# Kernel optimization log

Hardware: AMD Instinct MI355X
Metric: run time of the kernel (lower is better)

## Reference

```python
import jax, jax.numpy as jnp
import numpy as np
from jax import lax

T = 1.0      # terminal time
SIGMA = 1.0  # diffusion coefficient
N, D, P, M, H = 16384, 16, 8, 50, 128


def setup_inputs() -> dict:
    key = jax.random.key(0)
    ks = jax.random.split(key, 8)
    scale1 = 1.0 / np.sqrt(1 + D + P)
    scale2 = 1.0 / np.sqrt(H)
    return {
        "initial_states": jax.random.normal(ks[0], (N, D), jnp.float32),
        "initial_values": jax.random.normal(ks[1], (N,), jnp.float32),
        "observations": jax.random.normal(ks[2], (N, P), jnp.float32),
        "noise": jax.random.normal(ks[3], (M, N, D), jnp.float32),
        "W1": jax.random.normal(ks[4], (1 + D + P, H), jnp.float32) * scale1,
        "b1": jnp.zeros((H,), jnp.float32),
        "W2": jax.random.normal(ks[5], (H, H), jnp.float32) * scale2,
        "b2": jnp.zeros((H,), jnp.float32),
        "W3": jax.random.normal(ks[6], (H, D), jnp.float32) * scale2,
        "b3": jnp.zeros((D,), jnp.float32),
    }


def reference(initial_states, initial_values, observations, noise,
              W1, b1, W2, b2, W3, b3):
    """Euler-Maruyama rollout of simulate_SDEs: joint (X, V) SDE with
    per-step Z-network drift. drift b(X) = -X (OU process)."""
    m_steps = noise.shape[0]
    dt = jnp.asarray(T / m_steps, initial_states.dtype)
    sqrt_dt = jnp.sqrt(dt)
    times = jnp.arange(m_steps, dtype=initial_states.dtype) * dt  # time[m]

    def z_net(t, X, Y):
        tcol = jnp.full((X.shape[0], 1), t, X.dtype)
        h = jnp.concatenate([tcol, X, Y], axis=1)      # (N, 1+d+p)
        h = jax.nn.relu(h @ W1 + b1)
        h = jax.nn.relu(h @ W2 + b2)
        return h @ W3 + b3                             # (N, d)

    def step(carry, inp):
        X, V = carry
        eps, t = inp
        Wn = sqrt_dt * eps                             # Brownian increment
        Z = z_net(t, X, observations)
        drift_V = 0.5 * jnp.sum(Z * Z, axis=1)
        V = V + dt * drift_V + jnp.sum(Z * Wn, axis=1)
        X = X + dt * (-X) + SIGMA * Wn                 # b(X) = -X
        return (X, V), None

    (X, V), _ = lax.scan(step, (initial_states, initial_values), (noise, times))
    return X, V
```

## Files before the change

### kernel.cpp

```cpp
#include <hip/hip_runtime.h>

typedef __bf16   bf16x8 __attribute__((ext_vector_type(8)));
typedef float    f32x4  __attribute__((ext_vector_type(4)));
typedef float    f32x2  __attribute__((ext_vector_type(2)));
typedef uint32_t u32x4  __attribute__((ext_vector_type(4)));

constexpr int N_ = 16384;
constexpr int D_ = 16;
constexpr int P_ = 8;
constexpr int H_ = 128;
constexpr int M_ = 50;

__device__ __forceinline__ uint32_t pk_bf16(float a, float b) {
    uint32_t ua = __builtin_bit_cast(uint32_t, a) + 0x8000u;
    uint32_t ub = __builtin_bit_cast(uint32_t, b) + 0x8000u;
    return __builtin_amdgcn_perm(ub, ua, 0x07060302u);
}
__device__ __forceinline__ uint32_t pk_relu_bf16(float a, float b) {
    return pk_bf16(fmaxf(a, 0.0f), fmaxf(b, 0.0f));
}

__global__ __launch_bounds__(64, 1)
void sde_fused(const float* __restrict__ X0,
               const float* __restrict__ V0,
               const float* __restrict__ Yobs,
               const float* __restrict__ noise,
               const float* __restrict__ W1, const float* __restrict__ b1,
               const float* __restrict__ W2, const float* __restrict__ b2,
               const float* __restrict__ W3, const float* __restrict__ b3,
               float* __restrict__ out)
{
    const int lane = threadIdx.x;
    const int n    = lane & 15;
    const int q    = lane >> 4;
    const int gr   = blockIdx.x * 16 + n;

    const float dt   = 0.02f;
    const float sqdt = 0.1414213562373095f;

    bf16x8 w1f[8];
#pragma unroll
    for (int ct = 0; ct < 8; ++ct) {
        u32x4 u;
        u[0] = pk_bf16(W1[(1 + q * 4 + 0) * H_ + ct * 16 + n],
                       W1[(1 + q * 4 + 1) * H_ + ct * 16 + n]);
        u[1] = pk_bf16(W1[(1 + q * 4 + 2) * H_ + ct * 16 + n],
                       W1[(1 + q * 4 + 3) * H_ + ct * 16 + n]);
        u[2] = pk_bf16(W1[(17 + q * 2 + 0) * H_ + ct * 16 + n],
                       W1[(17 + q * 2 + 1) * H_ + ct * 16 + n]);
        u[3] = (q == 0) ? pk_bf16(b1[ct * 16 + n], W1[ct * 16 + n]) : 0u;
        w1f[ct] = __builtin_bit_cast(bf16x8, u);
    }
    bf16x8 w2f[8][4];
#pragma unroll
    for (int ct = 0; ct < 8; ++ct)
#pragma unroll
        for (int kt = 0; kt < 4; ++kt) {
            u32x4 u;
#pragma unroll
            for (int w = 0; w < 4; ++w) {
                int h0 = (kt * 2 + (w >> 1)) * 16 + q * 4 + (w & 1) * 2;
                u[w] = pk_bf16(W2[h0 * H_ + ct * 16 + n],
                               W2[(h0 + 1) * H_ + ct * 16 + n]);
            }
            w2f[ct][kt] = __builtin_bit_cast(bf16x8, u);
        }
    bf16x8 w3f[4];
#pragma unroll
    for (int kt = 0; kt < 4; ++kt) {
        u32x4 u;
#pragma unroll
        for (int w = 0; w < 4; ++w) {
            int h0 = (kt * 2 + (w >> 1)) * 16 + q * 4 + (w & 1) * 2;
            u[w] = pk_bf16(W3[h0 * D_ + n], W3[(h0 + 1) * D_ + n]);
        }
        w3f[kt] = __builtin_bit_cast(bf16x8, u);
    }
    f32x4 b2r[8];
#pragma unroll
    for (int ct = 0; ct < 8; ++ct)
#pragma unroll
        for (int r = 0; r < 4; ++r) b2r[ct][r] = b2[ct * 16 + q * 4 + r];
    f32x4 b3r;
#pragma unroll
    for (int r = 0; r < 4; ++r) b3r[r] = b3[q * 4 + r];

    f32x4 x = *(const f32x4*)&X0[gr * D_ + q * 4];
    f32x2 y2 = *(const f32x2*)&Yobs[gr * P_ + q * 2];
    const uint32_t yw = pk_bf16(y2[0], y2[1]);

    const float* npb = noise + (size_t)gr * D_ + q * 4;
    f32x4 e0 = *(const f32x4*)npb;
    f32x4 e1 = *(const f32x4*)(npb + (size_t)N_ * D_);
    float t = 0.0f;
    float vacc = 0.0f;

    for (int m = 0; m < M_; ++m) {
        int mp = (m + 2 < M_) ? (m + 2) : (M_ - 1);
        f32x4 e2 = *(const f32x4*)(npb + (size_t)mp * N_ * D_);

        u32x4 au;
        au[0] = pk_bf16(x[0], x[1]);
        au[1] = pk_bf16(x[2], x[3]);
        au[2] = yw;
        au[3] = (q == 0) ? pk_bf16(1.0f, t) : 0u;
        bf16x8 a0 = __builtin_bit_cast(bf16x8, au);

        f32x4 h1c[8];
#pragma unroll
        for (int ct = 0; ct < 8; ++ct)
            h1c[ct] = __builtin_amdgcn_mfma_f32_16x16x32_bf16(
                w1f[ct], a0, (f32x4){0.f, 0.f, 0.f, 0.f}, 0, 0, 0);

        bf16x8 h1b[4];
#pragma unroll
        for (int kt = 0; kt < 4; ++kt) {
            u32x4 u;
            u[0] = pk_relu_bf16(h1c[2 * kt][0], h1c[2 * kt][1]);
            u[1] = pk_relu_bf16(h1c[2 * kt][2], h1c[2 * kt][3]);
            u[2] = pk_relu_bf16(h1c[2 * kt + 1][0], h1c[2 * kt + 1][1]);
            u[3] = pk_relu_bf16(h1c[2 * kt + 1][2], h1c[2 * kt + 1][3]);
            h1b[kt] = __builtin_bit_cast(bf16x8, u);
        }

        f32x4 h2c[8];
#pragma unroll
        for (int ct = 0; ct < 8; ++ct) {
            f32x4 c = b2r[ct];
#pragma unroll
            for (int kt = 0; kt < 4; ++kt)
                c = __builtin_amdgcn_mfma_f32_16x16x32_bf16(w2f[ct][kt], h1b[kt], c, 0, 0, 0);
            h2c[ct] = c;
        }
        bf16x8 h2b[4];
#pragma unroll
        for (int kt = 0; kt < 4; ++kt) {
            u32x4 u;
            u[0] = pk_relu_bf16(h2c[2 * kt][0], h2c[2 * kt][1]);
            u[1] = pk_relu_bf16(h2c[2 * kt][2], h2c[2 * kt][3]);
            u[2] = pk_relu_bf16(h2c[2 * kt + 1][0], h2c[2 * kt + 1][1]);
            u[3] = pk_relu_bf16(h2c[2 * kt + 1][2], h2c[2 * kt + 1][3]);
            h2b[kt] = __builtin_bit_cast(bf16x8, u);
        }

        f32x4 za = __builtin_amdgcn_mfma_f32_16x16x32_bf16(w3f[0], h2b[0], b3r, 0, 0, 0);
        za = __builtin_amdgcn_mfma_f32_16x16x32_bf16(w3f[1], h2b[1], za, 0, 0, 0);
        f32x4 zb = __builtin_amdgcn_mfma_f32_16x16x32_bf16(
            w3f[2], h2b[2], (f32x4){0.f, 0.f, 0.f, 0.f}, 0, 0, 0);
        zb = __builtin_amdgcn_mfma_f32_16x16x32_bf16(w3f[3], h2b[3], zb, 0, 0, 0);

#pragma unroll
        for (int r = 0; r < 4; ++r) {
            float z  = za[r] + zb[r];
            float wn = sqdt * e0[r];
            vacc = fmaf(z, wn, fmaf(0.01f * z, z, vacc));
            x[r] = fmaf(x[r], 0.98f, wn);
        }

        e0 = e1; e1 = e2;
        t += dt;
    }

    float part = vacc;
    part += __shfl_xor(part, 16);
    part += __shfl_xor(part, 32);
    float v = V0[gr] + part;

    *(f32x4*)&out[gr * D_ + q * 4] = x;
    if (q == 0) out[N_ * D_ + gr] = v;
}

extern "C" void kernel_launch(void* const* d_in, const int* in_sizes, int n_in,
                              void* d_out, int out_size, void* d_ws, size_t ws_size,
                              hipStream_t stream)
{
    const float* X0 = (const float*)d_in[0];
    const float* V0 = (const float*)d_in[1];
    const float* Y  = (const float*)d_in[2];
    const float* nz = (const float*)d_in[3];
    const float* W1 = (const float*)d_in[4];
    const float* b1 = (const float*)d_in[5];
    const float* W2 = (const float*)d_in[6];
    const float* b2 = (const float*)d_in[7];
    const float* W3 = (const float*)d_in[8];
    const float* b3 = (const float*)d_in[9];
    float* out = (float*)d_out;

    sde_fused<<<N_ / 16, 64, 0, stream>>>(X0, V0, Y, nz, W1, b1, W2, b2, W3, b3, out);
}
```

Before: 139.6 us.

## Split hidden dimension across two waves with LDS exchange between MLP layers

Each 16-row block now uses two waves instead of one. Each wave computes half of the hidden columns for layers 1 and 2, then the halves are swapped through shared memory with a barrier so both waves hold full activations. This halves the per-wave MFMA chain and weight-register footprint, which is meant to cut per-step latency and raise occupancy. In exchange it adds two barriers and LDS round trips per time step, and both waves redundantly run layer 3 and the state update.

Measured after the change: 147.3 us. 1.06x slower.

```diff
diff --git a/kernel.cpp b/kernel.cpp
--- a/kernel.cpp
+++ b/kernel.cpp
@@ -20,7 +20,7 @@
     return pk_bf16(fmaxf(a, 0.0f), fmaxf(b, 0.0f));
 }
 
-__global__ __launch_bounds__(64, 1)
+__global__ __launch_bounds__(128, 2)
 void sde_fused(const float* __restrict__ X0,
                const float* __restrict__ V0,
                const float* __restrict__ Yobs,
@@ -30,17 +30,22 @@
                const float* __restrict__ W3, const float* __restrict__ b3,
                float* __restrict__ out)
 {
-    const int lane = threadIdx.x;
+    const int tid  = threadIdx.x;
+    const int lane = tid & 63;
+    const int wv   = tid >> 6;
     const int n    = lane & 15;
     const int q    = lane >> 4;
     const int gr   = blockIdx.x * 16 + n;
 
+    const int ct0 = wv * 4;
+
     const float dt   = 0.02f;
     const float sqdt = 0.1414213562373095f;
 
-    bf16x8 w1f[8];
-#pragma unroll
-    for (int ct = 0; ct < 8; ++ct) {
+    bf16x8 w1f[4];
+#pragma unroll
+    for (int c = 0; c < 4; ++c) {
+        const int ct = ct0 + c;
         u32x4 u;
         u[0] = pk_bf16(W1[(1 + q * 4 + 0) * H_ + ct * 16 + n],
                        W1[(1 + q * 4 + 1) * H_ + ct * 16 + n]);
@@ -49,41 +54,47 @@
         u[2] = pk_bf16(W1[(17 + q * 2 + 0) * H_ + ct * 16 + n],
                        W1[(17 + q * 2 + 1) * H_ + ct * 16 + n]);
         u[3] = (q == 0) ? pk_bf16(b1[ct * 16 + n], W1[ct * 16 + n]) : 0u;
-        w1f[ct] = __builtin_bit_cast(bf16x8, u);
-    }
-    bf16x8 w2f[8][4];
-#pragma unroll
-    for (int ct = 0; ct < 8; ++ct)
-#pragma unroll
-        for (int kt = 0; kt < 4; ++kt) {
+        w1f[c] = __builtin_bit_cast(bf16x8, u);
+    }
+    bf16x8 w2f[4][4];
+#pragma unroll
+    for (int cc = 0; cc < 4; ++cc) {
+        const int ct = ct0 + cc;
+#pragma unroll
+        for (int s = 0; s < 4; ++s) {
+            const int g = (s < 2) ? (2 * wv + s) : (2 * (wv ^ 1) + (s - 2));
             u32x4 u;
 #pragma unroll
             for (int w = 0; w < 4; ++w) {
-                int h0 = (kt * 2 + (w >> 1)) * 16 + q * 4 + (w & 1) * 2;
+                int h0 = (g * 2 + (w >> 1)) * 16 + q * 4 + (w & 1) * 2;
                 u[w] = pk_bf16(W2[h0 * H_ + ct * 16 + n],
                                W2[(h0 + 1) * H_ + ct * 16 + n]);
             }
-            w2f[ct][kt] = __builtin_bit_cast(bf16x8, u);
-        }
+            w2f[cc][s] = __builtin_bit_cast(bf16x8, u);
+        }
+    }
     bf16x8 w3f[4];
 #pragma unroll
-    for (int kt = 0; kt < 4; ++kt) {
+    for (int s = 0; s < 4; ++s) {
+        const int g = (s < 2) ? (2 * wv + s) : (2 * (wv ^ 1) + (s - 2));
         u32x4 u;
 #pragma unroll
         for (int w = 0; w < 4; ++w) {
-            int h0 = (kt * 2 + (w >> 1)) * 16 + q * 4 + (w & 1) * 2;
+            int h0 = (g * 2 + (w >> 1)) * 16 + q * 4 + (w & 1) * 2;
             u[w] = pk_bf16(W3[h0 * D_ + n], W3[(h0 + 1) * D_ + n]);
         }
-        w3f[kt] = __builtin_bit_cast(bf16x8, u);
-    }
-    f32x4 b2r[8];
-#pragma unroll
-    for (int ct = 0; ct < 8; ++ct)
-#pragma unroll
-        for (int r = 0; r < 4; ++r) b2r[ct][r] = b2[ct * 16 + q * 4 + r];
+        w3f[s] = __builtin_bit_cast(bf16x8, u);
+    }
+    f32x4 b2r[4];
+#pragma unroll
+    for (int cc = 0; cc < 4; ++cc)
+#pragma unroll
+        for (int r = 0; r < 4; ++r) b2r[cc][r] = b2[(ct0 + cc) * 16 + q * 4 + r];
     f32x4 b3r;
 #pragma unroll
     for (int r = 0; r < 4; ++r) b3r[r] = b3[q * 4 + r];
+
+    __shared__ bf16x8 xch[2][2][2][64];
 
     f32x4 x = *(const f32x4*)&X0[gr * D_ + q * 4];
     f32x2 y2 = *(const f32x2*)&Yobs[gr * P_ + q * 2];
@@ -106,48 +117,80 @@
         au[3] = (q == 0) ? pk_bf16(1.0f, t) : 0u;
         bf16x8 a0 = __builtin_bit_cast(bf16x8, au);
 
-        f32x4 h1c[8];
-#pragma unroll
-        for (int ct = 0; ct < 8; ++ct)
-            h1c[ct] = __builtin_amdgcn_mfma_f32_16x16x32_bf16(
-                w1f[ct], a0, (f32x4){0.f, 0.f, 0.f, 0.f}, 0, 0, 0);
-
-        bf16x8 h1b[4];
-#pragma unroll
-        for (int kt = 0; kt < 4; ++kt) {
-            u32x4 u;
-            u[0] = pk_relu_bf16(h1c[2 * kt][0], h1c[2 * kt][1]);
-            u[1] = pk_relu_bf16(h1c[2 * kt][2], h1c[2 * kt][3]);
-            u[2] = pk_relu_bf16(h1c[2 * kt + 1][0], h1c[2 * kt + 1][1]);
-            u[3] = pk_relu_bf16(h1c[2 * kt + 1][2], h1c[2 * kt + 1][3]);
-            h1b[kt] = __builtin_bit_cast(bf16x8, u);
-        }
-
-        f32x4 h2c[8];
-#pragma unroll
-        for (int ct = 0; ct < 8; ++ct) {
-            f32x4 c = b2r[ct];
-#pragma unroll
-            for (int kt = 0; kt < 4; ++kt)
-                c = __builtin_amdgcn_mfma_f32_16x16x32_bf16(w2f[ct][kt], h1b[kt], c, 0, 0, 0);
-            h2c[ct] = c;
-        }
-        bf16x8 h2b[4];
-#pragma unroll
-        for (int kt = 0; kt < 4; ++kt) {
-            u32x4 u;
-            u[0] = pk_relu_bf16(h2c[2 * kt][0], h2c[2 * kt][1]);
-            u[1] = pk_relu_bf16(h2c[2 * kt][2], h2c[2 * kt][3]);
-            u[2] = pk_relu_bf16(h2c[2 * kt + 1][0], h2c[2 * kt + 1][1]);
-            u[3] = pk_relu_bf16(h2c[2 * kt + 1][2], h2c[2 * kt + 1][3]);
-            h2b[kt] = __builtin_bit_cast(bf16x8, u);
-        }
-
-        f32x4 za = __builtin_amdgcn_mfma_f32_16x16x32_bf16(w3f[0], h2b[0], b3r, 0, 0, 0);
-        za = __builtin_amdgcn_mfma_f32_16x16x32_bf16(w3f[1], h2b[1], za, 0, 0, 0);
+        f32x4 h1c[4];
+#pragma unroll
+        for (int c = 0; c < 4; ++c)
+            h1c[c] = __builtin_amdgcn_mfma_f32_16x16x32_bf16(
+                w1f[c], a0, (f32x4){0.f, 0.f, 0.f, 0.f}, 0, 0, 0);
+
+        bf16x8 my0, my1;
+        {
+            u32x4 u;
+            u[0] = pk_relu_bf16(h1c[0][0], h1c[0][1]);
+            u[1] = pk_relu_bf16(h1c[0][2], h1c[0][3]);
+            u[2] = pk_relu_bf16(h1c[1][0], h1c[1][1]);
+            u[3] = pk_relu_bf16(h1c[1][2], h1c[1][3]);
+            my0 = __builtin_bit_cast(bf16x8, u);
+        }
+        {
+            u32x4 u;
+            u[0] = pk_relu_bf16(h1c[2][0], h1c[2][1]);
+            u[1] = pk_relu_bf16(h1c[2][2], h1c[2][3]);
+            u[2] = pk_relu_bf16(h1c[3][0], h1c[3][1]);
+            u[3] = pk_relu_bf16(h1c[3][2], h1c[3][3]);
+            my1 = __builtin_bit_cast(bf16x8, u);
+        }
+
+        xch[0][wv][0][lane] = my0;
+        xch[0][wv][1][lane] = my1;
+        asm volatile("s_waitcnt lgkmcnt(0)" ::: "memory");
+        __builtin_amdgcn_s_barrier();
+        __builtin_amdgcn_sched_barrier(0);
+        bf16x8 ot0 = xch[0][wv ^ 1][0][lane];
+        bf16x8 ot1 = xch[0][wv ^ 1][1][lane];
+
+        f32x4 h2c[4];
+#pragma unroll
+        for (int cc = 0; cc < 4; ++cc) {
+            f32x4 c = b2r[cc];
+            c = __builtin_amdgcn_mfma_f32_16x16x32_bf16(w2f[cc][0], my0, c, 0, 0, 0);
+            c = __builtin_amdgcn_mfma_f32_16x16x32_bf16(w2f[cc][1], my1, c, 0, 0, 0);
+            c = __builtin_amdgcn_mfma_f32_16x16x32_bf16(w2f[cc][2], ot0, c, 0, 0, 0);
+            c = __builtin_amdgcn_mfma_f32_16x16x32_bf16(w2f[cc][3], ot1, c, 0, 0, 0);
+            h2c[cc] = c;
+        }
+
+        bf16x8 m20, m21;
+        {
+            u32x4 u;
+            u[0] = pk_relu_bf16(h2c[0][0], h2c[0][1]);
+            u[1] = pk_relu_bf16(h2c[0][2], h2c[0][3]);
+            u[2] = pk_relu_bf16(h2c[1][0], h2c[1][1]);
+            u[3] = pk_relu_bf16(h2c[1][2], h2c[1][3]);
+            m20 = __builtin_bit_cast(bf16x8, u);
+        }
+        {
+            u32x4 u;
+            u[0] = pk_relu_bf16(h2c[2][0], h2c[2][1]);
+            u[1] = pk_relu_bf16(h2c[2][2], h2c[2][3]);
+            u[2] = pk_relu_bf16(h2c[3][0], h2c[3][1]);
+            u[3] = pk_relu_bf16(h2c[3][2], h2c[3][3]);
+            m21 = __builtin_bit_cast(bf16x8, u);
+        }
+
+        xch[1][wv][0][lane] = m20;
+        xch[1][wv][1][lane] = m21;
+        asm volatile("s_waitcnt lgkmcnt(0)" ::: "memory");
+        __builtin_amdgcn_s_barrier();
+        __builtin_amdgcn_sched_barrier(0);
+        bf16x8 o20 = xch[1][wv ^ 1][0][lane];
+        bf16x8 o21 = xch[1][wv ^ 1][1][lane];
+
+        f32x4 za = __builtin_amdgcn_mfma_f32_16x16x32_bf16(w3f[0], m20, b3r, 0, 0, 0);
+        za = __builtin_amdgcn_mfma_f32_16x16x32_bf16(w3f[1], m21, za, 0, 0, 0);
         f32x4 zb = __builtin_amdgcn_mfma_f32_16x16x32_bf16(
-            w3f[2], h2b[2], (f32x4){0.f, 0.f, 0.f, 0.f}, 0, 0, 0);
-        zb = __builtin_amdgcn_mfma_f32_16x16x32_bf16(w3f[3], h2b[3], zb, 0, 0, 0);
+            w3f[2], o20, (f32x4){0.f, 0.f, 0.f, 0.f}, 0, 0, 0);
+        zb = __builtin_amdgcn_mfma_f32_16x16x32_bf16(w3f[3], o21, zb, 0, 0, 0);
 
 #pragma unroll
         for (int r = 0; r < 4; ++r) {
@@ -164,10 +207,11 @@
     float part = vacc;
     part += __shfl_xor(part, 16);
     part += __shfl_xor(part, 32);
-    float v = V0[gr] + part;
-
-    *(f32x4*)&out[gr * D_ + q * 4] = x;
-    if (q == 0) out[N_ * D_ + gr] = v;
+
+    if (wv == 0) {
+        *(f32x4*)&out[gr * D_ + q * 4] = x;
+        if (q == 0) out[N_ * D_ + gr] = V0[gr] + part;
+    }
 }
 
 extern "C" void kernel_launch(void* const* d_in, const int* in_sizes, int n_in,
@@ -186,5 +230,5 @@
     const float* b3 = (const float*)d_in[9];
     float* out = (float*)d_out;
 
-    sde_fused<<<N_ / 16, 64, 0, stream>>>(X0, V0, Y, nz, W1, b1, W2, b2, W3, b3, out);
-}
+    sde_fused<<<N_ / 16, 128, 0, stream>>>(X0, V0, Y, nz, W1, b1, W2, b2, W3, b3, out);
+}
```

## Split time steps across two waves per sample group using closed-form X recurrence

Applied to the files above, without the earlier changes.

Each block now runs two wavefronts over the same 16 samples. The first handles steps 0-24. The second first replays the cheap X recurrence over the first 25 noise slices to get X at the midpoint, then runs the MLP for steps 25-49. The V partial sums are combined through shared memory, which halves the serial MLP chain per wave and doubles the number of waves available to hide MFMA latency. In exchange it reads the first half of the noise twice, adds a block barrier, and raises register pressure, since launch bounds allow two blocks of 128 threads.

After: 240.6 us. 72.4% more time.

```diff
diff --git a/kernel.cpp b/kernel.cpp
--- a/kernel.cpp
+++ b/kernel.cpp
@@ -20,7 +20,7 @@
     return pk_bf16(fmaxf(a, 0.0f), fmaxf(b, 0.0f));
 }
 
-__global__ __launch_bounds__(64, 1)
+__global__ __launch_bounds__(128, 2)
 void sde_fused(const float* __restrict__ X0,
                const float* __restrict__ V0,
                const float* __restrict__ Yobs,
@@ -30,7 +30,9 @@
                const float* __restrict__ W3, const float* __restrict__ b3,
                float* __restrict__ out)
 {
-    const int lane = threadIdx.x;
+    const int tid  = threadIdx.x;
+    const int lane = tid & 63;
+    const int half = tid >> 6;
     const int n    = lane & 15;
     const int q    = lane >> 4;
     const int gr   = blockIdx.x * 16 + n;
@@ -90,13 +92,27 @@
     const uint32_t yw = pk_bf16(y2[0], y2[1]);
 
     const float* npb = noise + (size_t)gr * D_ + q * 4;
-    f32x4 e0 = *(const f32x4*)npb;
-    f32x4 e1 = *(const f32x4*)(npb + (size_t)N_ * D_);
-    float t = 0.0f;
+
+    if (half == 1) {
+#pragma unroll 5
+        for (int m = 0; m < 25; ++m) {
+            f32x4 e = *(const f32x4*)(npb + (size_t)m * N_ * D_);
+#pragma unroll
+            for (int r = 0; r < 4; ++r)
+                x[r] = fmaf(x[r], 0.98f, sqdt * e[r]);
+        }
+    }
+
+    const int s0 = half * 25;
+    float t = half ? 0.5f : 0.0f;
+
+    f32x4 e0 = *(const f32x4*)(npb + (size_t)s0 * N_ * D_);
+    f32x4 e1 = *(const f32x4*)(npb + (size_t)(s0 + 1) * N_ * D_);
     float vacc = 0.0f;
 
-    for (int m = 0; m < M_; ++m) {
-        int mp = (m + 2 < M_) ? (m + 2) : (M_ - 1);
+    for (int i = 0; i < 25; ++i) {
+        const int m  = s0 + i;
+        const int mp = (m + 2 < M_) ? (m + 2) : (M_ - 1);
         f32x4 e2 = *(const f32x4*)(npb + (size_t)mp * N_ * D_);
 
         u32x4 au;
@@ -164,10 +180,14 @@
     float part = vacc;
     part += __shfl_xor(part, 16);
     part += __shfl_xor(part, 32);
-    float v = V0[gr] + part;
-
-    *(f32x4*)&out[gr * D_ + q * 4] = x;
-    if (q == 0) out[N_ * D_ + gr] = v;
+
+    __shared__ float vpart[16];
+    if (half == 0 && q == 0) vpart[n] = part;
+    __syncthreads();
+    if (half == 1) {
+        *(f32x4*)&out[gr * D_ + q * 4] = x;
+        if (q == 0) out[N_ * D_ + gr] = V0[gr] + vpart[n] + part;
+    }
 }
 
 extern "C" void kernel_launch(void* const* d_in, const int* in_sizes, int n_in,
@@ -186,5 +206,5 @@
     const float* b3 = (const float*)d_in[9];
     float* out = (float*)d_out;
 
-    sde_fused<<<N_ / 16, 64, 0, stream>>>(X0, V0, Y, nz, W1, b1, W2, b2, W3, b3, out);
-}
+    sde_fused<<<N_ / 16, 128, 0, stream>>>(X0, V0, Y, nz, W1, b1, W2, b2, W3, b3, out);
+}
```

## Software-pipeline layer-1 MFMA of next step and use hardware bf16 pack

Applied to the files above, without the earlier changes.

Restructures the time loop so the next step's X update and first-layer MFMAs are issued alongside the current step's layer-2/3 MFMAs. This breaks the serial dependency chain inside a single wave, since each block is only one wave with one block per launch-bound. It also replaces the manual add-and-permute bf16 packing with the v_cvt_pk_bf16_f32 instruction, which rounds to nearest even. The cost is higher register pressure from the extra h1cn accumulators, and the loop is now `unroll 1` with a peeled prologue and epilogue.

After: 139.3 us. About the same (-0.2%).

```diff
diff --git a/kernel.cpp b/kernel.cpp
--- a/kernel.cpp
+++ b/kernel.cpp
@@ -16,8 +16,13 @@
     uint32_t ub = __builtin_bit_cast(uint32_t, b) + 0x8000u;
     return __builtin_amdgcn_perm(ub, ua, 0x07060302u);
 }
-__device__ __forceinline__ uint32_t pk_relu_bf16(float a, float b) {
-    return pk_bf16(fmaxf(a, 0.0f), fmaxf(b, 0.0f));
+__device__ __forceinline__ uint32_t cvtpk(float a, float b) {
+    uint32_t r;
+    asm("v_cvt_pk_bf16_f32 %0, %1, %2" : "=v"(r) : "v"(a), "v"(b));
+    return r;
+}
+__device__ __forceinline__ uint32_t cvtpk_relu(float a, float b) {
+    return cvtpk(fmaxf(a, 0.0f), fmaxf(b, 0.0f));
 }
 
 __global__ __launch_bounds__(64, 1)
@@ -95,33 +100,50 @@
     float t = 0.0f;
     float vacc = 0.0f;
 
-    for (int m = 0; m < M_; ++m) {
-        int mp = (m + 2 < M_) ? (m + 2) : (M_ - 1);
-        f32x4 e2 = *(const f32x4*)(npb + (size_t)mp * N_ * D_);
-
+    bf16x8 h1b[4];
+    {
         u32x4 au;
-        au[0] = pk_bf16(x[0], x[1]);
-        au[1] = pk_bf16(x[2], x[3]);
+        au[0] = cvtpk(x[0], x[1]);
+        au[1] = cvtpk(x[2], x[3]);
         au[2] = yw;
-        au[3] = (q == 0) ? pk_bf16(1.0f, t) : 0u;
+        au[3] = (q == 0) ? cvtpk(1.0f, 0.0f) : 0u;
         bf16x8 a0 = __builtin_bit_cast(bf16x8, au);
-
         f32x4 h1c[8];
 #pragma unroll
         for (int ct = 0; ct < 8; ++ct)
             h1c[ct] = __builtin_amdgcn_mfma_f32_16x16x32_bf16(
                 w1f[ct], a0, (f32x4){0.f, 0.f, 0.f, 0.f}, 0, 0, 0);
-
-        bf16x8 h1b[4];
-#pragma unroll
-        for (int kt = 0; kt < 4; ++kt) {
-            u32x4 u;
-            u[0] = pk_relu_bf16(h1c[2 * kt][0], h1c[2 * kt][1]);
-            u[1] = pk_relu_bf16(h1c[2 * kt][2], h1c[2 * kt][3]);
-            u[2] = pk_relu_bf16(h1c[2 * kt + 1][0], h1c[2 * kt + 1][1]);
-            u[3] = pk_relu_bf16(h1c[2 * kt + 1][2], h1c[2 * kt + 1][3]);
+#pragma unroll
+        for (int kt = 0; kt < 4; ++kt) {
+            u32x4 u;
+            u[0] = cvtpk_relu(h1c[2 * kt][0], h1c[2 * kt][1]);
+            u[1] = cvtpk_relu(h1c[2 * kt][2], h1c[2 * kt][3]);
+            u[2] = cvtpk_relu(h1c[2 * kt + 1][0], h1c[2 * kt + 1][1]);
+            u[3] = cvtpk_relu(h1c[2 * kt + 1][2], h1c[2 * kt + 1][3]);
             h1b[kt] = __builtin_bit_cast(bf16x8, u);
         }
+    }
+
+#pragma unroll 1
+    for (int m = 0; m < M_ - 1; ++m) {
+        const int mp = (m + 2 < M_) ? (m + 2) : (M_ - 1);
+        f32x4 e2 = *(const f32x4*)(npb + (size_t)mp * N_ * D_);
+
+        f32x4 xn;
+#pragma unroll
+        for (int r = 0; r < 4; ++r) xn[r] = fmaf(x[r], 0.98f, sqdt * e0[r]);
+
+        u32x4 aun;
+        aun[0] = cvtpk(xn[0], xn[1]);
+        aun[1] = cvtpk(xn[2], xn[3]);
+        aun[2] = yw;
+        aun[3] = (q == 0) ? cvtpk(1.0f, t + dt) : 0u;
+        bf16x8 a0n = __builtin_bit_cast(bf16x8, aun);
+        f32x4 h1cn[8];
+#pragma unroll
+        for (int ct = 0; ct < 8; ++ct)
+            h1cn[ct] = __builtin_amdgcn_mfma_f32_16x16x32_bf16(
+                w1f[ct], a0n, (f32x4){0.f, 0.f, 0.f, 0.f}, 0, 0, 0);
 
         f32x4 h2c[8];
 #pragma unroll
@@ -129,17 +151,18 @@
             f32x4 c = b2r[ct];
 #pragma unroll
             for (int kt = 0; kt < 4; ++kt)
-                c = __builtin_amdgcn_mfma_f32_16x16x32_bf16(w2f[ct][kt], h1b[kt], c, 0, 0, 0);
+                c = __builtin_amdgcn_mfma_f32_16x16x32_bf16(
+                    w2f[ct][kt], h1b[kt], c, 0, 0, 0);
             h2c[ct] = c;
         }
         bf16x8 h2b[4];
 #pragma unroll
         for (int kt = 0; kt < 4; ++kt) {
             u32x4 u;
-            u[0] = pk_relu_bf16(h2c[2 * kt][0], h2c[2 * kt][1]);
-            u[1] = pk_relu_bf16(h2c[2 * kt][2], h2c[2 * kt][3]);
-            u[2] = pk_relu_bf16(h2c[2 * kt + 1][0], h2c[2 * kt + 1][1]);
-            u[3] = pk_relu_bf16(h2c[2 * kt + 1][2], h2c[2 * kt + 1][3]);
+            u[0] = cvtpk_relu(h2c[2 * kt][0], h2c[2 * kt][1]);
+            u[1] = cvtpk_relu(h2c[2 * kt][2], h2c[2 * kt][3]);
+            u[2] = cvtpk_relu(h2c[2 * kt + 1][0], h2c[2 * kt + 1][1]);
+            u[3] = cvtpk_relu(h2c[2 * kt + 1][2], h2c[2 * kt + 1][3]);
             h2b[kt] = __builtin_bit_cast(bf16x8, u);
         }
 
@@ -150,15 +173,59 @@
         zb = __builtin_amdgcn_mfma_f32_16x16x32_bf16(w3f[3], h2b[3], zb, 0, 0, 0);
 
 #pragma unroll
+        for (int kt = 0; kt < 4; ++kt) {
+            u32x4 u;
+            u[0] = cvtpk_relu(h1cn[2 * kt][0], h1cn[2 * kt][1]);
+            u[1] = cvtpk_relu(h1cn[2 * kt][2], h1cn[2 * kt][3]);
+            u[2] = cvtpk_relu(h1cn[2 * kt + 1][0], h1cn[2 * kt + 1][1]);
+            u[3] = cvtpk_relu(h1cn[2 * kt + 1][2], h1cn[2 * kt + 1][3]);
+            h1b[kt] = __builtin_bit_cast(bf16x8, u);
+        }
+
+#pragma unroll
+        for (int r = 0; r < 4; ++r) {
+            float z  = za[r] + zb[r];
+            float wn = sqdt * e0[r];
+            vacc = fmaf(z, wn, fmaf(0.01f * z, z, vacc));
+        }
+        x = xn;
+        e0 = e1; e1 = e2;
+        t += dt;
+    }
+
+    {
+        f32x4 h2c[8];
+#pragma unroll
+        for (int ct = 0; ct < 8; ++ct) {
+            f32x4 c = b2r[ct];
+#pragma unroll
+            for (int kt = 0; kt < 4; ++kt)
+                c = __builtin_amdgcn_mfma_f32_16x16x32_bf16(
+                    w2f[ct][kt], h1b[kt], c, 0, 0, 0);
+            h2c[ct] = c;
+        }
+        bf16x8 h2b[4];
+#pragma unroll
+        for (int kt = 0; kt < 4; ++kt) {
+            u32x4 u;
+            u[0] = cvtpk_relu(h2c[2 * kt][0], h2c[2 * kt][1]);
+            u[1] = cvtpk_relu(h2c[2 * kt][2], h2c[2 * kt][3]);
+            u[2] = cvtpk_relu(h2c[2 * kt + 1][0], h2c[2 * kt + 1][1]);
+            u[3] = cvtpk_relu(h2c[2 * kt + 1][2], h2c[2 * kt + 1][3]);
+            h2b[kt] = __builtin_bit_cast(bf16x8, u);
+        }
+        f32x4 za = __builtin_amdgcn_mfma_f32_16x16x32_bf16(w3f[0], h2b[0], b3r, 0, 0, 0);
+        za = __builtin_amdgcn_mfma_f32_16x16x32_bf16(w3f[1], h2b[1], za, 0, 0, 0);
+        f32x4 zb = __builtin_amdgcn_mfma_f32_16x16x32_bf16(
+            w3f[2], h2b[2], (f32x4){0.f, 0.f, 0.f, 0.f}, 0, 0, 0);
+        zb = __builtin_amdgcn_mfma_f32_16x16x32_bf16(w3f[3], h2b[3], zb, 0, 0, 0);
+#pragma unroll
         for (int r = 0; r < 4; ++r) {
             float z  = za[r] + zb[r];
             float wn = sqdt * e0[r];
             vacc = fmaf(z, wn, fmaf(0.01f * z, z, vacc));
             x[r] = fmaf(x[r], 0.98f, wn);
         }
-
-        e0 = e1; e1 = e2;
-        t += dt;
     }
 
     float part = vacc;
```
